# Kernel optimization log

Hardware: AMD Instinct MI355X
Metric: run time of the kernel (lower is better)

Reference implementation:

```python
import jax, jax.numpy as jnp
import numpy as np

N = 4096        # num_nodes
U = 64          # num_units
D = 64          # input_dim
B = 32          # batch
K = 2           # max_diffusion_step
M = K + 1       # num_matrices (1 support * K + identity)


def _build_support(seed=0):
    # random symmetric nonneg sparse adjacency (~avg degree 16), then scaled Laplacian
    rng = np.random.default_rng(seed)
    density = 16.0 / N
    mask = rng.random((N, N)) < density
    A = rng.random((N, N)).astype(np.float32) * mask
    A = np.maximum(A, A.T)
    np.fill_diagonal(A, 0.0)
    d = A.sum(axis=1)
    d_inv_sqrt = np.where(d > 0, 1.0 / np.sqrt(np.maximum(d, 1e-12)), 0.0)
    L = np.eye(N, dtype=np.float32) - (d_inv_sqrt[:, None] * A) * d_inv_sqrt[None, :]
    # scaled Laplacian with lambda_max ~= 2 (standard ChebNet approximation): L_s = 2/lmax * L - I
    return (L - np.eye(N, dtype=np.float32)).astype(np.float32)


def setup_inputs() -> dict:
    key = jax.random.key(0)
    k1, k2, k3, k4 = jax.random.split(key, 4)
    S = D + U  # concat(inputs, state) feature size = 128
    return {
        "inputs": jax.random.normal(k1, (B, N * D), dtype=jnp.float32),
        "hx": jax.random.normal(k2, (B, N * U), dtype=jnp.float32),
        "support": jnp.asarray(_build_support()),
        "W_ru": jax.random.normal(k3, (S * M, 2 * U), dtype=jnp.float32) * (2.0 / (S * M + 2 * U)) ** 0.5,
        "b_ru": jnp.ones((2 * U,), dtype=jnp.float32),  # bias_start=1.0 for GRU gates
        "W_c": jax.random.normal(k4, (S * M, U), dtype=jnp.float32) * (2.0 / (S * M + U)) ** 0.5,
        "b_c": jnp.zeros((U,), dtype=jnp.float32),
    }


def _gconv(support, x_in, state, W, b):
    # x_in: (B, N, D), state: (B, N, U)
    x0 = jnp.concatenate([x_in, state], axis=2)          # (B, N, S)
    S = x0.shape[2]
    x0 = x0.transpose(1, 2, 0).reshape(N, S * B)         # (N, S*B)
    xs = [x0]
    xk_m1, xk = x0, support @ x0                          # T_1 = L x
    xs.append(xk)
    for _ in range(K - 1):                                # Chebyshev recursion
        xk_p1 = 2.0 * (support @ xk) - xk_m1
        xs.append(xk_p1)
        xk_m1, xk = xk, xk_p1
    x = jnp.stack(xs, axis=0)                             # (M, N, S*B)
    x = x.reshape(M, N, S, B).transpose(3, 1, 2, 0)       # (B, N, S, M)
    x = x.reshape(B * N, S * M)
    return x @ W + b                                      # (B*N, out)


def reference(inputs, hx, support, W_ru, b_ru, W_c, b_c):
    x_in = inputs.reshape(B, N, D)
    h = hx.reshape(B, N, U)
    ru = jax.nn.sigmoid(_gconv(support, x_in, h, W_ru, b_ru)).reshape(B, N, 2 * U)
    r, u = jnp.split(ru, 2, axis=2)                       # reset, update gates
    c = jnp.tanh(_gconv(support, x_in, r * h, W_c, b_c)).reshape(B, N, U)
    new_h = u * h + (1.0 - u) * c
    return new_h.reshape(B, N * U)
```

## Files before the change

kernel.cpp:

```cpp
#include <hip/hip_runtime.h>

#define NN 4096
#define BB 32
#define UU 64
#define MAXNNZ 96

typedef float f32x4 __attribute__((ext_vector_type(4)));
typedef float f32x2 __attribute__((ext_vector_type(2)));
typedef short bf16x8 __attribute__((ext_vector_type(8)));
typedef unsigned short us8 __attribute__((ext_vector_type(8)));
typedef unsigned short us4 __attribute__((ext_vector_type(4)));

__device__ __forceinline__ float bf2f(unsigned short u) {
    return __uint_as_float(((unsigned)u) << 16);
}
__device__ __forceinline__ unsigned short f2bf(float f) {
    unsigned x = __float_as_uint(f);
    x += 0x7fffu + ((x >> 16) & 1u);
    return (unsigned short)(x >> 16);
}

__global__ void build_ell(const float* __restrict__ sup, int* __restrict__ cols,
                          float* __restrict__ vals, int* __restrict__ cnt) {
    int row  = blockIdx.x * 4 + (threadIdx.x >> 6);
    int lane = threadIdx.x & 63;
    const float* rp = sup + (size_t)row * NN;
    int base = 0;
    for (int ch = 0; ch < NN / 64; ++ch) {
        float v = rp[ch * 64 + lane];
        unsigned long long m = __ballot(v != 0.0f);
        int pos = __popcll(m & ((1ull << lane) - 1ull));
        if (v != 0.0f) {
            int idx = base + pos;
            if (idx < MAXNNZ) {
                cols[row * MAXNNZ + idx] = ch * 64 + lane;
                vals[row * MAXNNZ + idx] = v;
            }
        }
        base += __popcll(m);
    }
    if (lane == 0) cnt[row] = base < MAXNNZ ? base : MAXNNZ;
}

__global__ void build_x0(const float* __restrict__ inp, const float* __restrict__ hxp,
                         unsigned short* __restrict__ Xall) {
    size_t tt = (size_t)blockIdx.x * 256 + threadIdx.x;
    size_t e  = tt * 4;
    int half  = e >= (size_t)8388608;
    size_t id = e & 8388607ull;
    const float* src = half ? hxp : inp;
    float4 f = *(const float4*)(src + id);
    int d = (int)(id & 63);
    int n = (int)((id >> 6) & 4095);
    int b = (int)(id >> 18);
    us4 o;
    o[0] = f2bf(f.x); o[1] = f2bf(f.y); o[2] = f2bf(f.z); o[3] = f2bf(f.w);
    *(us4*)(Xall + (size_t)n * 4096 + (size_t)half * 2048 + b * 64 + d) = o;
}

__global__ void prep_w(const float* __restrict__ Wru, const float* __restrict__ Wc,
                       unsigned short* __restrict__ Wt1, unsigned short* __restrict__ Wt2) {
    int t = blockIdx.x * 256 + threadIdx.x;
    if (t < 49152) {
        int o = t / 384, f = t - o * 384;
        int s = f & 127, m = f >> 7;
        Wt1[t] = f2bf(Wru[(s * 3 + m) * 128 + o]);
    } else {
        int u = t - 49152;
        int o = u / 384, f = u - o * 384;
        int s = f & 127, m = f >> 7;
        Wt2[u] = f2bf(Wc[(s * 3 + m) * 64 + o]);
    }
}

template <bool CHEB>
__launch_bounds__(256)
__global__ void spmm_kernel(const int* __restrict__ cols, const float* __restrict__ vals,
                            const int* __restrict__ cnt, const unsigned short* __restrict__ X,
                            const unsigned short* __restrict__ Z0,
                            unsigned short* __restrict__ Y, int ncols) {
    int T = gridDim.x;
    int fid = blockIdx.x;
    int v = (fid & 7) * (T >> 3) + (fid >> 3);
    int chunk = v >> 10;
    int rg = v & 1023;
    int row = __builtin_amdgcn_readfirstlane(rg * 4 + (threadIdx.x >> 6));
    int lane = threadIdx.x & 63;
    int c = chunk * 512 + lane * 8;
    const int* cp = cols + row * MAXNNZ;
    const float* vp = vals + row * MAXNNZ;
    int kc = cnt[row];
    f32x2 acc0 = {0.f, 0.f}, acc1 = {0.f, 0.f}, acc2 = {0.f, 0.f}, acc3 = {0.f, 0.f};
    int k = 0;
    for (; k + 4 <= kc; k += 4) {
        int j0 = cp[k], j1 = cp[k + 1], j2 = cp[k + 2], j3 = cp[k + 3];
        float s0 = vp[k], s1 = vp[k + 1], s2 = vp[k + 2], s3 = vp[k + 3];
        us8 x0 = *(const us8*)(X + (size_t)j0 * ncols + c);
        us8 x1 = *(const us8*)(X + (size_t)j1 * ncols + c);
        us8 x2 = *(const us8*)(X + (size_t)j2 * ncols + c);
        us8 x3 = *(const us8*)(X + (size_t)j3 * ncols + c);
        f32x2 w0 = {s0, s0}, w1 = {s1, s1}, w2 = {s2, s2}, w3 = {s3, s3};
        const unsigned* p0 = (const unsigned*)&x0;
        const unsigned* p1 = (const unsigned*)&x1;
        const unsigned* p2 = (const unsigned*)&x2;
        const unsigned* p3 = (const unsigned*)&x3;
#pragma unroll
        for (int i = 0; i < 4; ++i) {
            f32x2* ac = i == 0 ? &acc0 : (i == 1 ? &acc1 : (i == 2 ? &acc2 : &acc3));
            f32x2 xv;
            xv.x = __uint_as_float(p0[i] << 16); xv.y = __uint_as_float(p0[i] & 0xffff0000u);
            *ac = __builtin_elementwise_fma(w0, xv, *ac);
            xv.x = __uint_as_float(p1[i] << 16); xv.y = __uint_as_float(p1[i] & 0xffff0000u);
            *ac = __builtin_elementwise_fma(w1, xv, *ac);
            xv.x = __uint_as_float(p2[i] << 16); xv.y = __uint_as_float(p2[i] & 0xffff0000u);
            *ac = __builtin_elementwise_fma(w2, xv, *ac);
            xv.x = __uint_as_float(p3[i] << 16); xv.y = __uint_as_float(p3[i] & 0xffff0000u);
            *ac = __builtin_elementwise_fma(w3, xv, *ac);
        }
    }
    for (; k < kc; ++k) {
        int j = cp[k];
        float s = vp[k];
        f32x2 w = {s, s};
        us8 x = *(const us8*)(X + (size_t)j * ncols + c);
        const unsigned* p = (const unsigned*)&x;
#pragma unroll
        for (int i = 0; i < 4; ++i) {
            f32x2* ac = i == 0 ? &acc0 : (i == 1 ? &acc1 : (i == 2 ? &acc2 : &acc3));
            f32x2 xv;
            xv.x = __uint_as_float(p[i] << 16); xv.y = __uint_as_float(p[i] & 0xffff0000u);
            *ac = __builtin_elementwise_fma(w, xv, *ac);
        }
    }
    float a[8] = {acc0.x, acc0.y, acc1.x, acc1.y, acc2.x, acc2.y, acc3.x, acc3.y};
    if (CHEB) {
        us8 z = __builtin_nontemporal_load((const us8*)(Z0 + (size_t)row * ncols + c));
        const unsigned* pz = (const unsigned*)&z;
#pragma unroll
        for (int i = 0; i < 4; ++i) {
            a[2 * i]     = 2.f * a[2 * i]     - __uint_as_float(pz[i] << 16);
            a[2 * i + 1] = 2.f * a[2 * i + 1] - __uint_as_float(pz[i] & 0xffff0000u);
        }
    }
    us8 o;
#pragma unroll
    for (int i = 0; i < 8; ++i) o[i] = f2bf(a[i]);
    __builtin_nontemporal_store(o, (us8*)(Y + (size_t)row * ncols + c));
}

template <bool GATE>
__launch_bounds__(256)
__global__ void gemm_kernel(
    const unsigned short* __restrict__ in0, const unsigned short* __restrict__ in1,
    const unsigned short* __restrict__ in2,
    const unsigned short* __restrict__ st0, const unsigned short* __restrict__ st1,
    const unsigned short* __restrict__ st2, int stStride,
    const unsigned short* __restrict__ Wt, const float* __restrict__ bias,
    const float* __restrict__ hx, unsigned short* __restrict__ ubuf,
    unsigned short* __restrict__ x2st, float* __restrict__ outp) {
    constexpr int OC = GATE ? 128 : 64;
    constexpr int MF = GATE ? 8 : 4;
    __shared__ __align__(16) unsigned short A_lds[128 * 72];
    __shared__ __align__(16) unsigned short W_lds[OC * 72];
    const int t = threadIdx.x;
    const int w = t >> 6, l = t & 63;
    const int bid = blockIdx.x;
    const int b = bid >> 5;
    const int n0 = (bid & 31) * 128;
    const int rowBaseW = GATE ? 0 : ((w >> 1) * 64);
    const int colBaseW = GATE ? (w * 32) : ((w & 1) * 32);
    f32x4 acc[MF][2];
#pragma unroll
    for (int i = 0; i < MF; ++i)
#pragma unroll
        for (int j = 0; j < 2; ++j)
#pragma unroll
            for (int r2 = 0; r2 < 4; ++r2) acc[i][j][r2] = 0.f;

#pragma unroll
    for (int kk2 = 0; kk2 < 6; ++kk2) {
        const int m = kk2 >> 1;
        const bool stateReg = (kk2 & 1);
        const unsigned short* src =
            stateReg ? (m == 0 ? st0 : (m == 1 ? st1 : st2))
                     : (m == 0 ? in0 : (m == 1 ? in1 : in2));
        const int stride = stateReg ? stStride : NN;
        const int colb = b * 64;
        __syncthreads();
        {
            int i = t >> 1;
            int ho = (t & 1) * 32;
            const unsigned short* s = src + (size_t)(n0 + i) * stride + colb + ho;
            us8 v0 = *(const us8*)(s);
            us8 v1 = *(const us8*)(s + 8);
            us8 v2 = *(const us8*)(s + 16);
            us8 v3 = *(const us8*)(s + 24);
            unsigned short* d = &A_lds[i * 72 + ho];
            *(us8*)(d) = v0; *(us8*)(d + 8) = v1;
            *(us8*)(d + 16) = v2; *(us8*)(d + 24) = v3;
        }
        {
            int o = t >> 1;
            if (o < OC) {
                int ho = (t & 1) * 32;
                const unsigned short* s = Wt + o * 384 + kk2 * 64 + ho;
                us8 v0 = *(const us8*)(s);
                us8 v1 = *(const us8*)(s + 8);
                us8 v2 = *(const us8*)(s + 16);
                us8 v3 = *(const us8*)(s + 24);
                unsigned short* d = &W_lds[o * 72 + ho];
                *(us8*)(d) = v0; *(us8*)(d + 8) = v1;
                *(us8*)(d + 16) = v2; *(us8*)(d + 24) = v3;
            }
        }
        __syncthreads();
#pragma unroll
        for (int ss = 0; ss < 2; ++ss) {
            const int kb = ss * 32 + (l >> 4) * 8;
            bf16x8 bf0 = *(const bf16x8*)(&W_lds[(colBaseW + (l & 15)) * 72 + kb]);
            bf16x8 bf1 = *(const bf16x8*)(&W_lds[(colBaseW + 16 + (l & 15)) * 72 + kb]);
#pragma unroll
            for (int mf = 0; mf < MF; ++mf) {
                int r = rowBaseW + mf * 16 + (l & 15);
                bf16x8 a = *(const bf16x8*)(&A_lds[r * 72 + kb]);
                acc[mf][0] = __builtin_amdgcn_mfma_f32_16x16x32_bf16(a, bf0, acc[mf][0], 0, 0, 0);
                acc[mf][1] = __builtin_amdgcn_mfma_f32_16x16x32_bf16(a, bf1, acc[mf][1], 0, 0, 0);
            }
        }
    }
    const int l4 = (l >> 4) * 4;
    const int lc = l & 15;
    if (GATE) {
#pragma unroll
        for (int mf = 0; mf < MF; ++mf) {
#pragma unroll
            for (int nf = 0; nf < 2; ++nf) {
                int col = colBaseW + nf * 16 + lc;
#pragma unroll
                for (int rr = 0; rr < 4; ++rr) {
                    int nn = n0 + mf * 16 + l4 + rr;
                    float vv = acc[mf][nf][rr] + bias[col];
                    float s = 1.f / (1.f + __expf(-vv));
                    if (col < 64) {
                        float h = hx[(size_t)b * (NN * UU) + (size_t)nn * UU + col];
                        x2st[(size_t)nn * 2048 + b * 64 + col] = f2bf(s * h);
                    } else {
                        ubuf[(size_t)b * (NN * UU) + (size_t)nn * UU + (col - 64)] = f2bf(s);
                    }
                }
            }
        }
    } else {
#pragma unroll
        for (int mf = 0; mf < MF; ++mf) {
#pragma unroll
            for (int nf = 0; nf < 2; ++nf) {
                int col = colBaseW + nf * 16 + lc;
#pragma unroll
                for (int rr = 0; rr < 4; ++rr) {
                    int nn = n0 + rowBaseW + mf * 16 + l4 + rr;
                    size_t idx = (size_t)b * (NN * UU) + (size_t)nn * UU + col;
                    float cc = tanhf(acc[mf][nf][rr] + bias[col]);
                    float u = bf2f(ubuf[idx]);
                    float h = hx[idx];
                    outp[idx] = u * h + (1.f - u) * cc;
                }
            }
        }
    }
}

extern "C" void kernel_launch(void* const* d_in, const int* in_sizes, int n_in,
                              void* d_out, int out_size, void* d_ws, size_t ws_size,
                              hipStream_t stream) {
    const float* inputs  = (const float*)d_in[0];
    const float* hx      = (const float*)d_in[1];
    const float* support = (const float*)d_in[2];
    const float* W_ru    = (const float*)d_in[3];
    const float* b_ru    = (const float*)d_in[4];
    const float* W_c     = (const float*)d_in[5];
    const float* b_c     = (const float*)d_in[6];
    float* out = (float*)d_out;

    char* ws = (char*)d_ws;
    size_t off = 0;
    auto alloc = [&](size_t bytes) -> char* {
        char* p = ws + off;
        off = (off + bytes + 255) & ~(size_t)255;
        return p;
    };
    int*            colsI = (int*)  alloc((size_t)NN * MAXNNZ * 4);
    float*          valsF = (float*)alloc((size_t)NN * MAXNNZ * 4);
    int*            cntI  = (int*)  alloc((size_t)NN * 4);
    unsigned short* Wt1   = (unsigned short*)alloc(128 * 384 * 2);
    unsigned short* Wt2   = (unsigned short*)alloc(64 * 384 * 2);
    unsigned short* Xall  = (unsigned short*)alloc((size_t)NN * 4096 * 2);
    unsigned short* Z1    = (unsigned short*)alloc((size_t)NN * 4096 * 2);
    unsigned short* Z2    = (unsigned short*)alloc((size_t)NN * 4096 * 2);
    unsigned short* X2st  = (unsigned short*)alloc((size_t)NN * 2048 * 2);
    unsigned short* Z1st  = (unsigned short*)alloc((size_t)NN * 2048 * 2);
    unsigned short* Z2st  = (unsigned short*)alloc((size_t)NN * 2048 * 2);
    unsigned short* ubuf  = (unsigned short*)alloc((size_t)BB * NN * UU * 2);
    if (off > ws_size) return;

    build_ell<<<1024, 256, 0, stream>>>(support, colsI, valsF, cntI);
    build_x0<<<16384, 256, 0, stream>>>(inputs, hx, Xall);
    prep_w<<<288, 256, 0, stream>>>(W_ru, W_c, Wt1, Wt2);

    spmm_kernel<false><<<8192, 256, 0, stream>>>(colsI, valsF, cntI, Xall, Xall, Z1, 4096);
    spmm_kernel<true><<<8192, 256, 0, stream>>>(colsI, valsF, cntI, Z1, Xall, Z2, 4096);
    gemm_kernel<true><<<1024, 256, 0, stream>>>(Xall, Z1, Z2, Xall + 2048, Z1 + 2048,
                                                Z2 + 2048, 4096, Wt1, b_ru, hx, ubuf,
                                                X2st, nullptr);
    spmm_kernel<false><<<4096, 256, 0, stream>>>(colsI, valsF, cntI, X2st, X2st, Z1st, 2048);
    spmm_kernel<true><<<4096, 256, 0, stream>>>(colsI, valsF, cntI, Z1st, X2st, Z2st, 2048);
    gemm_kernel<false><<<1024, 256, 0, stream>>>(Xall, Z1, Z2, X2st, Z1st, Z2st, 2048,
                                                 Wt2, b_c, hx, ubuf, nullptr, out);
}
```

Baseline: 312.5 us.

## Prefetch next GEMM K-slice into registers, remap tiles to node-major rows, unroll SpMM by 8

The GEMM kernels now load the next K-slice of A and W into registers while MFMAs run on the current LDS tile, which is a software-pipelined register prefetch. Each block now covers 4 nodes across all 32 batches instead of 128 nodes for one batch, so every wave reads one contiguous 64-element row segment. The epilogue index math is updated to match. The SpMM inner loop is unrolled to 8 gathers per iteration to keep more memory loads in flight, at the cost of higher register pressure.

```diff
diff --git a/kernel.cpp b/kernel.cpp
--- a/kernel.cpp
+++ b/kernel.cpp
@@ -92,30 +92,27 @@
     int kc = cnt[row];
     f32x2 acc0 = {0.f, 0.f}, acc1 = {0.f, 0.f}, acc2 = {0.f, 0.f}, acc3 = {0.f, 0.f};
     int k = 0;
-    for (; k + 4 <= kc; k += 4) {
-        int j0 = cp[k], j1 = cp[k + 1], j2 = cp[k + 2], j3 = cp[k + 3];
-        float s0 = vp[k], s1 = vp[k + 1], s2 = vp[k + 2], s3 = vp[k + 3];
-        us8 x0 = *(const us8*)(X + (size_t)j0 * ncols + c);
-        us8 x1 = *(const us8*)(X + (size_t)j1 * ncols + c);
-        us8 x2 = *(const us8*)(X + (size_t)j2 * ncols + c);
-        us8 x3 = *(const us8*)(X + (size_t)j3 * ncols + c);
-        f32x2 w0 = {s0, s0}, w1 = {s1, s1}, w2 = {s2, s2}, w3 = {s3, s3};
-        const unsigned* p0 = (const unsigned*)&x0;
-        const unsigned* p1 = (const unsigned*)&x1;
-        const unsigned* p2 = (const unsigned*)&x2;
-        const unsigned* p3 = (const unsigned*)&x3;
-#pragma unroll
-        for (int i = 0; i < 4; ++i) {
-            f32x2* ac = i == 0 ? &acc0 : (i == 1 ? &acc1 : (i == 2 ? &acc2 : &acc3));
+    for (; k + 8 <= kc; k += 8) {
+        us8 xx[8];
+        float ss[8];
+#pragma unroll
+        for (int u = 0; u < 8; ++u) {
+            xx[u] = *(const us8*)(X + (size_t)cp[k + u] * ncols + c);
+            ss[u] = vp[k + u];
+        }
+#pragma unroll
+        for (int u = 0; u < 8; ++u) {
+            f32x2 w = {ss[u], ss[u]};
+            const unsigned* p = (const unsigned*)&xx[u];
             f32x2 xv;
-            xv.x = __uint_as_float(p0[i] << 16); xv.y = __uint_as_float(p0[i] & 0xffff0000u);
-            *ac = __builtin_elementwise_fma(w0, xv, *ac);
-            xv.x = __uint_as_float(p1[i] << 16); xv.y = __uint_as_float(p1[i] & 0xffff0000u);
-            *ac = __builtin_elementwise_fma(w1, xv, *ac);
-            xv.x = __uint_as_float(p2[i] << 16); xv.y = __uint_as_float(p2[i] & 0xffff0000u);
-            *ac = __builtin_elementwise_fma(w2, xv, *ac);
-            xv.x = __uint_as_float(p3[i] << 16); xv.y = __uint_as_float(p3[i] & 0xffff0000u);
-            *ac = __builtin_elementwise_fma(w3, xv, *ac);
+            xv.x = __uint_as_float(p[0] << 16); xv.y = __uint_as_float(p[0] & 0xffff0000u);
+            acc0 = __builtin_elementwise_fma(w, xv, acc0);
+            xv.x = __uint_as_float(p[1] << 16); xv.y = __uint_as_float(p[1] & 0xffff0000u);
+            acc1 = __builtin_elementwise_fma(w, xv, acc1);
+            xv.x = __uint_as_float(p[2] << 16); xv.y = __uint_as_float(p[2] & 0xffff0000u);
+            acc2 = __builtin_elementwise_fma(w, xv, acc2);
+            xv.x = __uint_as_float(p[3] << 16); xv.y = __uint_as_float(p[3] & 0xffff0000u);
+            acc3 = __builtin_elementwise_fma(w, xv, acc3);
         }
     }
     for (; k < kc; ++k) {
@@ -124,13 +121,15 @@
         f32x2 w = {s, s};
         us8 x = *(const us8*)(X + (size_t)j * ncols + c);
         const unsigned* p = (const unsigned*)&x;
-#pragma unroll
-        for (int i = 0; i < 4; ++i) {
-            f32x2* ac = i == 0 ? &acc0 : (i == 1 ? &acc1 : (i == 2 ? &acc2 : &acc3));
-            f32x2 xv;
-            xv.x = __uint_as_float(p[i] << 16); xv.y = __uint_as_float(p[i] & 0xffff0000u);
-            *ac = __builtin_elementwise_fma(w, xv, *ac);
-        }
+        f32x2 xv;
+        xv.x = __uint_as_float(p[0] << 16); xv.y = __uint_as_float(p[0] & 0xffff0000u);
+        acc0 = __builtin_elementwise_fma(w, xv, acc0);
+        xv.x = __uint_as_float(p[1] << 16); xv.y = __uint_as_float(p[1] & 0xffff0000u);
+        acc1 = __builtin_elementwise_fma(w, xv, acc1);
+        xv.x = __uint_as_float(p[2] << 16); xv.y = __uint_as_float(p[2] & 0xffff0000u);
+        acc2 = __builtin_elementwise_fma(w, xv, acc2);
+        xv.x = __uint_as_float(p[3] << 16); xv.y = __uint_as_float(p[3] & 0xffff0000u);
+        acc3 = __builtin_elementwise_fma(w, xv, acc3);
     }
     float a[8] = {acc0.x, acc0.y, acc1.x, acc1.y, acc2.x, acc2.y, acc3.x, acc3.y};
     if (CHEB) {
@@ -151,10 +150,10 @@
 template <bool GATE>
 __launch_bounds__(256)
 __global__ void gemm_kernel(
-    const unsigned short* __restrict__ in0, const unsigned short* __restrict__ in1,
-    const unsigned short* __restrict__ in2,
-    const unsigned short* __restrict__ st0, const unsigned short* __restrict__ st1,
-    const unsigned short* __restrict__ st2, int stStride,
+    const unsigned short* __restrict__ s0, const unsigned short* __restrict__ s1,
+    const unsigned short* __restrict__ s2, const unsigned short* __restrict__ s3,
+    const unsigned short* __restrict__ s4, const unsigned short* __restrict__ s5,
+    int strideSt,
     const unsigned short* __restrict__ Wt, const float* __restrict__ bias,
     const float* __restrict__ hx, unsigned short* __restrict__ ubuf,
     unsigned short* __restrict__ x2st, float* __restrict__ outp) {
@@ -164,9 +163,11 @@
     __shared__ __align__(16) unsigned short W_lds[OC * 72];
     const int t = threadIdx.x;
     const int w = t >> 6, l = t & 63;
-    const int bid = blockIdx.x;
-    const int b = bid >> 5;
-    const int n0 = (bid & 31) * 128;
+    const int n0 = blockIdx.x * 4;
+    const int dn = w;
+    const int q = l;
+    const int o = t >> 1;
+    const int wq = t & 1;
     const int rowBaseW = GATE ? 0 : ((w >> 1) * 64);
     const int colBaseW = GATE ? (w * 32) : ((w & 1) * 32);
     f32x4 acc[MF][2];
@@ -177,43 +178,46 @@
 #pragma unroll
             for (int r2 = 0; r2 < 4; ++r2) acc[i][j][r2] = 0.f;
 
+    us8 avC[4], wvC[4], avN[4], wvN[4];
+    {
+        const unsigned short* a = s0 + (size_t)(n0 + dn) * NN + q * 32;
+        avC[0] = *(const us8*)(a);      avC[1] = *(const us8*)(a + 8);
+        avC[2] = *(const us8*)(a + 16); avC[3] = *(const us8*)(a + 24);
+        if (o < OC) {
+            const unsigned short* ww = Wt + o * 384 + wq * 32;
+            wvC[0] = *(const us8*)(ww);      wvC[1] = *(const us8*)(ww + 8);
+            wvC[2] = *(const us8*)(ww + 16); wvC[3] = *(const us8*)(ww + 24);
+        }
+    }
+
 #pragma unroll
     for (int kk2 = 0; kk2 < 6; ++kk2) {
-        const int m = kk2 >> 1;
-        const bool stateReg = (kk2 & 1);
-        const unsigned short* src =
-            stateReg ? (m == 0 ? st0 : (m == 1 ? st1 : st2))
-                     : (m == 0 ? in0 : (m == 1 ? in1 : in2));
-        const int stride = stateReg ? stStride : NN;
-        const int colb = b * 64;
         __syncthreads();
         {
-            int i = t >> 1;
-            int ho = (t & 1) * 32;
-            const unsigned short* s = src + (size_t)(n0 + i) * stride + colb + ho;
-            us8 v0 = *(const us8*)(s);
-            us8 v1 = *(const us8*)(s + 8);
-            us8 v2 = *(const us8*)(s + 16);
-            us8 v3 = *(const us8*)(s + 24);
-            unsigned short* d = &A_lds[i * 72 + ho];
-            *(us8*)(d) = v0; *(us8*)(d + 8) = v1;
-            *(us8*)(d + 16) = v2; *(us8*)(d + 24) = v3;
-        }
-        {
-            int o = t >> 1;
+            unsigned short* d = &A_lds[(dn * 32 + (q >> 1)) * 72 + (q & 1) * 32];
+            *(us8*)(d) = avC[0]; *(us8*)(d + 8) = avC[1];
+            *(us8*)(d + 16) = avC[2]; *(us8*)(d + 24) = avC[3];
             if (o < OC) {
-                int ho = (t & 1) * 32;
-                const unsigned short* s = Wt + o * 384 + kk2 * 64 + ho;
-                us8 v0 = *(const us8*)(s);
-                us8 v1 = *(const us8*)(s + 8);
-                us8 v2 = *(const us8*)(s + 16);
-                us8 v3 = *(const us8*)(s + 24);
-                unsigned short* d = &W_lds[o * 72 + ho];
-                *(us8*)(d) = v0; *(us8*)(d + 8) = v1;
-                *(us8*)(d + 16) = v2; *(us8*)(d + 24) = v3;
+                unsigned short* dw = &W_lds[o * 72 + wq * 32];
+                *(us8*)(dw) = wvC[0]; *(us8*)(dw + 8) = wvC[1];
+                *(us8*)(dw + 16) = wvC[2]; *(us8*)(dw + 24) = wvC[3];
             }
         }
         __syncthreads();
+        if (kk2 < 5) {
+            const int kn = kk2 + 1;
+            const unsigned short* src =
+                kn == 1 ? s1 : (kn == 2 ? s2 : (kn == 3 ? s3 : (kn == 4 ? s4 : s5)));
+            const int stride = (kn & 1) ? strideSt : NN;
+            const unsigned short* a = src + (size_t)(n0 + dn) * stride + q * 32;
+            avN[0] = *(const us8*)(a);      avN[1] = *(const us8*)(a + 8);
+            avN[2] = *(const us8*)(a + 16); avN[3] = *(const us8*)(a + 24);
+            if (o < OC) {
+                const unsigned short* ww = Wt + o * 384 + kn * 64 + wq * 32;
+                wvN[0] = *(const us8*)(ww);      wvN[1] = *(const us8*)(ww + 8);
+                wvN[2] = *(const us8*)(ww + 16); wvN[3] = *(const us8*)(ww + 24);
+            }
+        }
 #pragma unroll
         for (int ss = 0; ss < 2; ++ss) {
             const int kb = ss * 32 + (l >> 4) * 8;
@@ -227,7 +231,12 @@
                 acc[mf][1] = __builtin_amdgcn_mfma_f32_16x16x32_bf16(a, bf1, acc[mf][1], 0, 0, 0);
             }
         }
-    }
+        if (kk2 < 5) {
+#pragma unroll
+            for (int i = 0; i < 4; ++i) { avC[i] = avN[i]; wvC[i] = wvN[i]; }
+        }
+    }
+
     const int l4 = (l >> 4) * 4;
     const int lc = l & 15;
     if (GATE) {
@@ -238,7 +247,9 @@
                 int col = colBaseW + nf * 16 + lc;
 #pragma unroll
                 for (int rr = 0; rr < 4; ++rr) {
-                    int nn = n0 + mf * 16 + l4 + rr;
+                    int r = mf * 16 + l4 + rr;
+                    int nn = n0 + (r >> 5);
+                    int b = r & 31;
                     float vv = acc[mf][nf][rr] + bias[col];
                     float s = 1.f / (1.f + __expf(-vv));
                     if (col < 64) {
@@ -258,7 +269,9 @@
                 int col = colBaseW + nf * 16 + lc;
 #pragma unroll
                 for (int rr = 0; rr < 4; ++rr) {
-                    int nn = n0 + rowBaseW + mf * 16 + l4 + rr;
+                    int r = rowBaseW + mf * 16 + l4 + rr;
+                    int nn = n0 + (r >> 5);
+                    int b = r & 31;
                     size_t idx = (size_t)b * (NN * UU) + (size_t)nn * UU + col;
                     float cc = tanhf(acc[mf][nf][rr] + bias[col]);
                     float u = bf2f(ubuf[idx]);
@@ -309,11 +322,11 @@
 
     spmm_kernel<false><<<8192, 256, 0, stream>>>(colsI, valsF, cntI, Xall, Xall, Z1, 4096);
     spmm_kernel<true><<<8192, 256, 0, stream>>>(colsI, valsF, cntI, Z1, Xall, Z2, 4096);
-    gemm_kernel<true><<<1024, 256, 0, stream>>>(Xall, Z1, Z2, Xall + 2048, Z1 + 2048,
-                                                Z2 + 2048, 4096, Wt1, b_ru, hx, ubuf,
-                                                X2st, nullptr);
+    gemm_kernel<true><<<1024, 256, 0, stream>>>(Xall, Xall + 2048, Z1, Z1 + 2048,
+                                                Z2, Z2 + 2048, 4096, Wt1, b_ru, hx,
+                                                ubuf, X2st, nullptr);
     spmm_kernel<false><<<4096, 256, 0, stream>>>(colsI, valsF, cntI, X2st, X2st, Z1st, 2048);
     spmm_kernel<true><<<4096, 256, 0, stream>>>(colsI, valsF, cntI, Z1st, X2st, Z2st, 2048);
-    gemm_kernel<false><<<1024, 256, 0, stream>>>(Xall, Z1, Z2, X2st, Z1st, Z2st, 2048,
+    gemm_kernel<false><<<1024, 256, 0, stream>>>(Xall, X2st, Z1, Z1st, Z2, Z2st, 2048,
                                                  Wt2, b_c, hx, ubuf, nullptr, out);
 }
```

After: 324.6 us. +3.9%, slower.
